# Kernel tuning notes

Measured on AMD Instinct MI355X. Metric: run time of the kernel, lower is better.

## Reference

```python
import jax, jax.numpy as jnp
import numpy as np

B, NP, N, C, H = 16, 512, 1024, 1024, 16
HD = C // H
HID = 4 * C
EPS = 1e-5


def _layernorm(x, g, b):
    mu = jnp.mean(x, axis=-1, keepdims=True)
    var = jnp.mean(jnp.square(x - mu), axis=-1, keepdims=True)
    return (x - mu) * jax.lax.rsqrt(var + EPS) * g + b


def setup_inputs() -> dict:
    key = jax.random.key(0)
    ks = jax.random.split(key, 12)
    x = jax.random.normal(ks[0], (B, NP, C), dtype=jnp.float32)
    cache_k = jax.random.normal(ks[1], (B, H, N, HD), dtype=jnp.float32)
    cache_v = jax.random.normal(ks[2], (B, H, N, HD), dtype=jnp.float32)
    # update_mask: exactly NP active (to-be-updated) token slots per batch row
    scores = jax.random.uniform(ks[3], (B, N))
    top = jnp.argsort(scores, axis=1)[:, :NP]
    update_mask = jnp.zeros((B, N), dtype=bool).at[jnp.arange(B)[:, None], top].set(True)
    s = 0.02
    qkv_w = jax.random.normal(ks[4], (C, 3 * C), dtype=jnp.float32) * s
    qkv_b = jnp.zeros((3 * C,), dtype=jnp.float32)
    proj_w = jax.random.normal(ks[5], (C, C), dtype=jnp.float32) * s
    proj_b = jnp.zeros((C,), dtype=jnp.float32)
    n1_g = jnp.ones((C,), dtype=jnp.float32)
    n1_b = jnp.zeros((C,), dtype=jnp.float32)
    n2_g = jnp.ones((C,), dtype=jnp.float32)
    n2_b = jnp.zeros((C,), dtype=jnp.float32)
    fc1_w = jax.random.normal(ks[6], (C, HID), dtype=jnp.float32) * s
    fc1_b = jnp.zeros((HID,), dtype=jnp.float32)
    fc2_w = jax.random.normal(ks[7], (HID, C), dtype=jnp.float32) * s
    fc2_b = jnp.zeros((C,), dtype=jnp.float32)
    return dict(x=x, cache_k=cache_k, cache_v=cache_v, update_mask=update_mask,
                qkv_w=qkv_w, qkv_b=qkv_b, proj_w=proj_w, proj_b=proj_b,
                n1_g=n1_g, n1_b=n1_b, n2_g=n2_g, n2_b=n2_b,
                fc1_w=fc1_w, fc1_b=fc1_b, fc2_w=fc2_w, fc2_b=fc2_b)


def reference(x, cache_k, cache_v, update_mask, qkv_w, qkv_b, proj_w, proj_b,
              n1_g, n1_b, n2_g, n2_b, fc1_w, fc1_b, fc2_w, fc2_b):
    Bq, Np, Cd = x.shape
    h = _layernorm(x, n1_g, n1_b)
    qkv = (h @ qkv_w + qkv_b).reshape(Bq, Np, 3, H, HD)
    q, k, v = jnp.moveaxis(qkv, 2, 0)               # each [B, Np, H, HD]
    q = jnp.swapaxes(q, 1, 2)                       # [B, H, Np, HD]
    k = jnp.swapaxes(k, 1, 2)
    v = jnp.swapaxes(v, 1, 2)
    # masked_scatter_: i-th new token -> i-th masked slot (row-uniform mask count)
    idx = jnp.argsort(jnp.logical_not(update_mask), axis=1)[:, :Np]  # [B, Np]
    k_full = jax.vmap(lambda c, i, kn: c.at[:, i, :].set(kn))(cache_k, idx, k)
    v_full = jax.vmap(lambda c, i, vn: c.at[:, i, :].set(vn))(cache_v, idx, v)
    scale = HD ** -0.5
    attn = jnp.einsum('bhqd,bhkd->bhqk', q * scale, k_full)  # [B,H,Np,N]
    attn = jax.nn.softmax(attn, axis=-1)
    o = jnp.einsum('bhqk,bhkd->bhqd', attn, v_full)
    o = jnp.swapaxes(o, 1, 2).reshape(Bq, Np, Cd)
    o = o @ proj_w + proj_b
    x = x + o
    h2 = _layernorm(x, n2_g, n2_b)
    mlp = jax.nn.gelu(h2 @ fc1_w + fc1_b, approximate=False) @ fc2_w + fc2_b
    return x + mlp
```

## Files before the change

kernel.cpp:

```cpp
#include <hip/hip_runtime.h>
#include <hip/hip_bf16.h>
#include <math.h>

#define Bd   16
#define NPd  512
#define Nd   1024
#define Cd   1024
#define Hd   16
#define HDd  64
#define HIDd 4096
#define EPSd 1e-5f

typedef unsigned short u16;
typedef __bf16 bf16x8 __attribute__((ext_vector_type(8)));
typedef float  f32x4  __attribute__((ext_vector_type(4)));

__device__ __forceinline__ u16 f2bf(float f) {
    unsigned int u = __builtin_bit_cast(unsigned int, f);
    u = u + 0x7fffu + ((u >> 16) & 1u);
    return (u16)(u >> 16);
}

__device__ __forceinline__ void async_load16(const void* g, void* l) {
    __builtin_amdgcn_global_load_lds(
        (const __attribute__((address_space(1))) void*)(uintptr_t)g,
        (__attribute__((address_space(3))) void*)(unsigned int)(uintptr_t)l,
        16, 0, 0);
}

__global__ __launch_bounds__(256) void build_src(const void* __restrict__ mask_raw,
                                                 int* __restrict__ src) {
    const int b = blockIdx.x;
    const int t = threadIdx.x;
    const unsigned char* m8 = (const unsigned char*)mask_raw;
    const int* m32 = (const int*)mask_raw;

    int c = 0;
    #pragma unroll
    for (int i = 0; i < 4; i++) c += (m8[b * Nd + t * 4 + i] != 0) ? 1 : 0;
    #pragma unroll
    for (int off = 1; off < 64; off <<= 1) c += __shfl_xor(c, off);
    __shared__ int warr[4];
    if ((t & 63) == 0) warr[t >> 6] = c;
    __syncthreads();
    const int c8 = warr[0] + warr[1] + warr[2] + warr[3];
    const bool use8 = (c8 == NPd);

    int f[4];
    #pragma unroll
    for (int i = 0; i < 4; i++) {
        const int n = t * 4 + i;
        f[i] = use8 ? (m8[b * Nd + n] != 0) : (m32[b * Nd + n] != 0);
    }
    const int loc = f[0] + f[1] + f[2] + f[3];

    int sc_ = loc;
    #pragma unroll
    for (int off = 1; off < 64; off <<= 1) {
        const int u = __shfl_up(sc_, off);
        if ((t & 63) >= off) sc_ += u;
    }
    __shared__ int wtot[4];
    __syncthreads();
    if ((t & 63) == 63) wtot[t >> 6] = sc_;
    __syncthreads();
    int base = 0;
    for (int w = 0; w < (t >> 6); w++) base += wtot[w];

    int run = base + sc_ - loc;
    #pragma unroll
    for (int i = 0; i < 4; i++) {
        const int n = t * 4 + i;
        src[b * Nd + n] = f[i] ? run : -1;
        run += f[i];
    }
}

__global__ __launch_bounds__(256) void ln_kernel(const float* __restrict__ x,
                                                 const float* __restrict__ g,
                                                 const float* __restrict__ bb,
                                                 u16* __restrict__ out) {
    const int row = blockIdx.x;
    const int t = threadIdx.x;
    const float* xr = x + (size_t)row * Cd;
    const float4 v = *(const float4*)(xr + t * 4);
    float s = v.x + v.y + v.z + v.w;
    float q = v.x * v.x + v.y * v.y + v.z * v.z + v.w * v.w;
    #pragma unroll
    for (int off = 1; off < 64; off <<= 1) {
        s += __shfl_xor(s, off);
        q += __shfl_xor(q, off);
    }
    __shared__ float ss[4], qq[4];
    if ((t & 63) == 0) { ss[t >> 6] = s; qq[t >> 6] = q; }
    __syncthreads();
    s = ss[0] + ss[1] + ss[2] + ss[3];
    q = qq[0] + qq[1] + qq[2] + qq[3];
    const float mu = s * (1.0f / Cd);
    const float var = q * (1.0f / Cd) - mu * mu;
    const float rs = rsqrtf(var + EPSd);
    const float4 gv = *(const float4*)(g + t * 4);
    const float4 bv = *(const float4*)(bb + t * 4);
    ushort4 r;
    r.x = f2bf((v.x - mu) * rs * gv.x + bv.x);
    r.y = f2bf((v.y - mu) * rs * gv.y + bv.y);
    r.z = f2bf((v.z - mu) * rs * gv.z + bv.z);
    r.w = f2bf((v.w - mu) * rs * gv.w + bv.w);
    *(ushort4*)(out + (size_t)row * Cd + t * 4) = r;
}

__global__ __launch_bounds__(256) void conv_t(const float* __restrict__ W,
                                              u16* __restrict__ Wt,
                                              int K, int N) {
    __shared__ float tile[32][33];
    const int k0 = blockIdx.y * 32;
    const int n0 = blockIdx.x * 32;
    const int t = threadIdx.x;
    const int row = t >> 3, c4 = (t & 7) * 4;
    const float4 v = *(const float4*)(W + (size_t)(k0 + row) * N + n0 + c4);
    tile[row][c4 + 0] = v.x;
    tile[row][c4 + 1] = v.y;
    tile[row][c4 + 2] = v.z;
    tile[row][c4 + 3] = v.w;
    __syncthreads();
    ushort4 o;
    o.x = f2bf(tile[c4 + 0][row]);
    o.y = f2bf(tile[c4 + 1][row]);
    o.z = f2bf(tile[c4 + 2][row]);
    o.w = f2bf(tile[c4 + 3][row]);
    *(ushort4*)(Wt + (size_t)(n0 + row) * K + k0 + c4) = o;
}

template <int EPI, typename OUT_T>
__global__ __launch_bounds__(256) void gemm_mfma(const u16* __restrict__ A,
                                                 const u16* __restrict__ Wt,
                                                 const float* __restrict__ bias,
                                                 const float* __restrict__ res,
                                                 OUT_T* __restrict__ out,
                                                 int K, int Nn) {
    __shared__ u16 As[128 * 32];
    __shared__ u16 Bs[128 * 32];

    const int t = threadIdx.x;
    const int L = t & 63;
    const int w = t >> 6;
    const int wm = w >> 1, wn = w & 1;
    const int m0 = blockIdx.y * 128;
    const int n0 = blockIdx.x * 128;

    const int srow = 32 * w + (L >> 2);
    const int scol = (L & 3) * 8;
    const u16* ap0 = A  + (size_t)(m0 + srow) * K + scol;
    const u16* ap1 = ap0 + (size_t)16 * K;
    const u16* bp0 = Wt + (size_t)(n0 + srow) * K + scol;
    const u16* bp1 = bp0 + (size_t)16 * K;
    u16* alds0 = As + w * 1024;
    u16* alds1 = alds0 + 512;
    u16* blds0 = Bs + w * 1024;
    u16* blds1 = blds0 + 512;

    f32x4 acc[4][4];
    const f32x4 zero = {0.f, 0.f, 0.f, 0.f};
    #pragma unroll
    for (int i = 0; i < 4; i++)
        #pragma unroll
        for (int j = 0; j < 4; j++) acc[i][j] = zero;

    const int frag_off = (L & 15) * 32 + (L >> 4) * 8;

    for (int kt = 0; kt < K; kt += 32) {
        __syncthreads();
        async_load16(ap0 + kt, alds0);
        async_load16(ap1 + kt, alds1);
        async_load16(bp0 + kt, blds0);
        async_load16(bp1 + kt, blds1);
        __syncthreads();

        bf16x8 a[4], b[4];
        #pragma unroll
        for (int i = 0; i < 4; i++) {
            a[i] = *(const bf16x8*)&As[(wm * 64 + i * 16) * 32 + frag_off];
            b[i] = *(const bf16x8*)&Bs[(wn * 64 + i * 16) * 32 + frag_off];
        }
        #pragma unroll
        for (int i = 0; i < 4; i++)
            #pragma unroll
            for (int j = 0; j < 4; j++)
                acc[i][j] = __builtin_amdgcn_mfma_f32_16x16x32_bf16(a[i], b[j], acc[i][j], 0, 0, 0);
    }

    const int cn = n0 + wn * 64 + (L & 15);
    const int cm = m0 + wm * 64 + (L >> 4) * 4;
    #pragma unroll
    for (int i = 0; i < 4; i++) {
        #pragma unroll
        for (int j = 0; j < 4; j++) {
            const int nn = cn + j * 16;
            const float bv = bias[nn];
            #pragma unroll
            for (int r = 0; r < 4; r++) {
                const int mm = cm + i * 16 + r;
                float v = acc[i][j][r] + bv;
                if (EPI == 2) v = 0.5f * v * (1.0f + erff(v * 0.70710678118654752f));
                if (EPI == 1) v += res[(size_t)mm * Nn + nn];
                if constexpr (sizeof(OUT_T) == 2) out[(size_t)mm * Nn + nn] = (OUT_T)f2bf(v);
                else out[(size_t)mm * Nn + nn] = v;
            }
        }
    }
}

__global__ __launch_bounds__(256) void kv_cast(const u16* __restrict__ qkv,
                                               const float* __restrict__ ck,
                                               const float* __restrict__ cv,
                                               const int* __restrict__ srcArr,
                                               u16* __restrict__ Kb,
                                               u16* __restrict__ Vtb) {
    const int id = blockIdx.x;
    const int nt = id & 15, hh = (id >> 4) & 15, b = id >> 8;
    const int t = threadIdx.x;
    __shared__ u16 Vl[64][72];

    const int row = t >> 2;
    const int dd = (t & 3) * 16;
    const int n = nt * 64 + row;
    const int sidx = srcArr[b * Nd + n];

    u16 kv16[16], vv16[16];
    if (sidx >= 0) {
        const u16* kp = qkv + (size_t)(b * NPd + sidx) * 3072 + Cd + hh * 64 + dd;
        const u16* vp = kp + Cd;
        *(ulonglong2*)&kv16[0] = *(const ulonglong2*)kp;
        *(ulonglong2*)&kv16[8] = *(const ulonglong2*)(kp + 8);
        *(ulonglong2*)&vv16[0] = *(const ulonglong2*)vp;
        *(ulonglong2*)&vv16[8] = *(const ulonglong2*)(vp + 8);
    } else {
        const float* kp = ck + ((size_t)((b * Hd + hh) * Nd + n)) * HDd + dd;
        const float* vp = cv + ((size_t)((b * Hd + hh) * Nd + n)) * HDd + dd;
        #pragma unroll
        for (int c = 0; c < 4; c++) {
            const float4 kc4 = *(const float4*)(kp + c * 4);
            const float4 vc4 = *(const float4*)(vp + c * 4);
            kv16[c * 4 + 0] = f2bf(kc4.x); kv16[c * 4 + 1] = f2bf(kc4.y);
            kv16[c * 4 + 2] = f2bf(kc4.z); kv16[c * 4 + 3] = f2bf(kc4.w);
            vv16[c * 4 + 0] = f2bf(vc4.x); vv16[c * 4 + 1] = f2bf(vc4.y);
            vv16[c * 4 + 2] = f2bf(vc4.z); vv16[c * 4 + 3] = f2bf(vc4.w);
        }
    }

    u16* ko = Kb + ((size_t)((b * Hd + hh) * Nd + n)) * HDd + dd;
    *(ulonglong2*)ko = *(ulonglong2*)&kv16[0];
    *(ulonglong2*)(ko + 8) = *(ulonglong2*)&kv16[8];

    #pragma unroll
    for (int i = 0; i < 16; i++) Vl[row][dd + i] = vv16[i];
    __syncthreads();

    const int d = t >> 2, nc = (t & 3) * 16;
    u16 ov[16];
    #pragma unroll
    for (int i = 0; i < 16; i++) ov[i] = Vl[nc + i][d];
    u16* vo = Vtb + ((size_t)((b * Hd + hh) * HDd + d)) * Nd + nt * 64 + nc;
    *(ulonglong2*)vo = *(ulonglong2*)&ov[0];
    *(ulonglong2*)(vo + 8) = *(ulonglong2*)&ov[8];
}

__global__ __launch_bounds__(256) void attn_mfma(const u16* __restrict__ qkv,
                                                 const u16* __restrict__ Kb,
                                                 const u16* __restrict__ Vtb,
                                                 u16* __restrict__ attno) {
    const int bh = blockIdx.x;
    const int qt = blockIdx.y;
    const int b = bh >> 4, hh = bh & 15;
    const int t = threadIdx.x;
    const int L = t & 63;
    const int w = t >> 6;

    __shared__ u16 Qs[4096];
    __shared__ u16 Ks[4096];
    __shared__ u16 Vs[4096];
    __shared__ u16 Ps[4][16 * 72];

    const size_t kbase = (size_t)((b * Hd + hh) * Nd) * HDd;
    const size_t vbase = (size_t)((b * Hd + hh) * HDd) * Nd;

    #pragma unroll
    for (int j = 0; j < 2; j++) {
        const int row = 16 * w + 8 * j + (L >> 3);
        const int ch = (L & 7) ^ (row & 7);
        const u16* g = qkv + (size_t)(b * NPd + qt * 64 + row) * 3072 + hh * 64 + ch * 8;
        async_load16(g, Qs + (16 * w + 8 * j) * 64);
    }

    f32x4 acc[4];
    const f32x4 zero = {0.f, 0.f, 0.f, 0.f};
    #pragma unroll
    for (int nb = 0; nb < 4; nb++) acc[nb] = zero;
    float m_run[4] = {-INFINITY, -INFINITY, -INFINITY, -INFINITY};
    float l_run[4] = {0.f, 0.f, 0.f, 0.f};

    for (int kt = 0; kt < 16; kt++) {
        __syncthreads();
        #pragma unroll
        for (int j = 0; j < 2; j++) {
            const int row = 16 * w + 8 * j + (L >> 3);
            const int ch = (L & 7) ^ (row & 7);
            async_load16(Kb + kbase + (size_t)(kt * 64 + row) * 64 + ch * 8,
                         Ks + (16 * w + 8 * j) * 64);
            async_load16(Vtb + vbase + (size_t)row * Nd + kt * 64 + ch * 8,
                         Vs + (16 * w + 8 * j) * 64);
        }
        __syncthreads();

        const int qrow = 16 * w + (L & 15);
        const bf16x8 aq0 = *(const bf16x8*)&Qs[qrow * 64 + (((L >> 4)     ^ (L & 7)) * 8)];
        const bf16x8 aq1 = *(const bf16x8*)&Qs[qrow * 64 + (((4 + (L >> 4)) ^ (L & 7)) * 8)];

        f32x4 s[4];
        #pragma unroll
        for (int kb = 0; kb < 4; kb++) {
            const int krow = kb * 16 + (L & 15);
            const bf16x8 bk0 = *(const bf16x8*)&Ks[krow * 64 + (((L >> 4)     ^ (L & 7)) * 8)];
            const bf16x8 bk1 = *(const bf16x8*)&Ks[krow * 64 + (((4 + (L >> 4)) ^ (L & 7)) * 8)];
            s[kb] = __builtin_amdgcn_mfma_f32_16x16x32_bf16(aq0, bk0, zero, 0, 0, 0);
            s[kb] = __builtin_amdgcn_mfma_f32_16x16x32_bf16(aq1, bk1, s[kb], 0, 0, 0);
        }

        float al[4];
        float pb[4][4];
        #pragma unroll
        for (int r = 0; r < 4; r++) {
            float m = fmaxf(fmaxf(s[0][r], s[1][r]), fmaxf(s[2][r], s[3][r])) * 0.125f;
            m = fmaxf(m, __shfl_xor(m, 1));
            m = fmaxf(m, __shfl_xor(m, 2));
            m = fmaxf(m, __shfl_xor(m, 4));
            m = fmaxf(m, __shfl_xor(m, 8));
            const float mn = fmaxf(m_run[r], m);
            al[r] = __expf(m_run[r] - mn);
            m_run[r] = mn;
        }
        float ps[4] = {0.f, 0.f, 0.f, 0.f};
        #pragma unroll
        for (int kb = 0; kb < 4; kb++)
            #pragma unroll
            for (int r = 0; r < 4; r++) {
                const float p = __expf(s[kb][r] * 0.125f - m_run[r]);
                pb[kb][r] = p;
                ps[r] += p;
            }
        #pragma unroll
        for (int r = 0; r < 4; r++) {
            ps[r] += __shfl_xor(ps[r], 1);
            ps[r] += __shfl_xor(ps[r], 2);
            ps[r] += __shfl_xor(ps[r], 4);
            ps[r] += __shfl_xor(ps[r], 8);
            l_run[r] = l_run[r] * al[r] + ps[r];
        }
        #pragma unroll
        for (int nb = 0; nb < 4; nb++)
            #pragma unroll
            for (int r = 0; r < 4; r++) acc[nb][r] *= al[r];

        u16* pw = &Ps[w][0];
        #pragma unroll
        for (int kb = 0; kb < 4; kb++)
            #pragma unroll
            for (int r = 0; r < 4; r++)
                pw[((L >> 4) * 4 + r) * 72 + kb * 16 + (L & 15)] = f2bf(pb[kb][r]);

        const bf16x8 ap0 = *(const bf16x8*)&Ps[w][(L & 15) * 72 +      (L >> 4) * 8];
        const bf16x8 ap1 = *(const bf16x8*)&Ps[w][(L & 15) * 72 + 32 + (L >> 4) * 8];
        #pragma unroll
        for (int nb = 0; nb < 4; nb++) {
            const int drow = nb * 16 + (L & 15);
            const bf16x8 bv0 = *(const bf16x8*)&Vs[drow * 64 + (((L >> 4)     ^ (L & 7)) * 8)];
            const bf16x8 bv1 = *(const bf16x8*)&Vs[drow * 64 + (((4 + (L >> 4)) ^ (L & 7)) * 8)];
            acc[nb] = __builtin_amdgcn_mfma_f32_16x16x32_bf16(ap0, bv0, acc[nb], 0, 0, 0);
            acc[nb] = __builtin_amdgcn_mfma_f32_16x16x32_bf16(ap1, bv1, acc[nb], 0, 0, 0);
        }
    }

    float inv[4];
    #pragma unroll
    for (int r = 0; r < 4; r++) inv[r] = 1.0f / l_run[r];
    #pragma unroll
    for (int nb = 0; nb < 4; nb++)
        #pragma unroll
        for (int r = 0; r < 4; r++) {
            const int q = qt * 64 + w * 16 + (L >> 4) * 4 + r;
            const int d = nb * 16 + (L & 15);
            attno[(size_t)(b * NPd + q) * Cd + hh * 64 + d] = f2bf(acc[nb][r] * inv[r]);
        }
}

extern "C" void kernel_launch(void* const* d_in, const int* in_sizes, int n_in,
                              void* d_out, int out_size, void* d_ws, size_t ws_size,
                              hipStream_t stream) {
    const float* x       = (const float*)d_in[0];
    const float* cache_k = (const float*)d_in[1];
    const float* cache_v = (const float*)d_in[2];
    const void*  mask    = d_in[3];
    const float* qkv_w   = (const float*)d_in[4];
    const float* qkv_b   = (const float*)d_in[5];
    const float* proj_w  = (const float*)d_in[6];
    const float* proj_b  = (const float*)d_in[7];
    const float* n1_g    = (const float*)d_in[8];
    const float* n1_b    = (const float*)d_in[9];
    const float* n2_g    = (const float*)d_in[10];
    const float* n2_b    = (const float*)d_in[11];
    const float* fc1_w   = (const float*)d_in[12];
    const float* fc1_b   = (const float*)d_in[13];
    const float* fc2_w   = (const float*)d_in[14];
    const float* fc2_b   = (const float*)d_in[15];
    float* out = (float*)d_out;

    const size_t MR = (size_t)Bd * NPd;
    char* ws = (char*)d_ws;
    int*   srcArr = (int*)ws;
    float* x2     = (float*)(ws + 65536);
    u16*   h      = (u16*)(x2 + MR * Cd);
    u16*   attno  = h + MR * Cd;
    u16*   qkv    = attno + MR * Cd;
    u16*   Kb     = qkv + MR * 3 * Cd;
    u16*   Vtb    = Kb + (size_t)Bd * Hd * Nd * HDd;
    u16*   m1     = qkv;
    u16*   qkv_wt = Vtb + (size_t)Bd * Hd * Nd * HDd;
    u16*   proj_wt= qkv_wt + (size_t)3 * Cd * Cd;
    u16*   fc1_wt = proj_wt + (size_t)Cd * Cd;
    u16*   fc2_wt = fc1_wt + (size_t)Cd * HIDd;

    build_src<<<Bd, 256, 0, stream>>>(mask, srcArr);
    conv_t<<<dim3(3 * Cd / 32, Cd / 32),  256, 0, stream>>>(qkv_w,  qkv_wt,  Cd,   3 * Cd);
    conv_t<<<dim3(Cd / 32, Cd / 32),      256, 0, stream>>>(proj_w, proj_wt, Cd,   Cd);
    conv_t<<<dim3(HIDd / 32, Cd / 32),    256, 0, stream>>>(fc1_w,  fc1_wt,  Cd,   HIDd);
    conv_t<<<dim3(Cd / 32, HIDd / 32),    256, 0, stream>>>(fc2_w,  fc2_wt,  HIDd, Cd);

    ln_kernel<<<MR, 256, 0, stream>>>(x, n1_g, n1_b, h);
    gemm_mfma<0, u16><<<dim3(3 * Cd / 128, MR / 128), 256, 0, stream>>>(h, qkv_wt, qkv_b, nullptr, qkv, Cd, 3 * Cd);
    kv_cast<<<Bd * Hd * (Nd / 64), 256, 0, stream>>>(qkv, cache_k, cache_v, srcArr, Kb, Vtb);
    attn_mfma<<<dim3(Bd * Hd, NPd / 64), 256, 0, stream>>>(qkv, Kb, Vtb, attno);
    gemm_mfma<1, float><<<dim3(Cd / 128, MR / 128), 256, 0, stream>>>(attno, proj_wt, proj_b, x, x2, Cd, Cd);
    ln_kernel<<<MR, 256, 0, stream>>>(x2, n2_g, n2_b, h);
    gemm_mfma<2, u16><<<dim3(HIDd / 128, MR / 128), 256, 0, stream>>>(h, fc1_wt, fc1_b, nullptr, m1, Cd, HIDd);
    gemm_mfma<1, float><<<dim3(Cd / 128, MR / 128), 256, 0, stream>>>(m1, fc2_wt, fc2_b, x2, out, HIDd, Cd);
}
```

Baseline: 703.3 us.

## Split-K the proj and fc2 GEMMs and fuse partial reduction with LayerNorm

The projection and fc2 GEMMs are launched with two K-slices, so each gets twice as many blocks, and write fp32 partials into reused workspace buffers. A new reduce kernel adds the two partials, bias and residual, and for the projection also computes LN2 in the same pass, replacing the separate ln_kernel. This aims to improve CU occupancy on the narrow N=1024 GEMMs. In exchange it writes and reads extra fp32 partial buffers and aliases them onto dead workspace regions.

```diff
diff --git a/kernel.cpp b/kernel.cpp
--- a/kernel.cpp
+++ b/kernel.cpp
@@ -208,6 +208,143 @@
             }
         }
     }
+}
+
+__global__ __launch_bounds__(256) void gemm_mfma_sk(const u16* __restrict__ A,
+                                                    const u16* __restrict__ Wt,
+                                                    float* __restrict__ part0,
+                                                    float* __restrict__ part1,
+                                                    int Kstride, int KL, int Nn) {
+    __shared__ u16 As[128 * 32];
+    __shared__ u16 Bs[128 * 32];
+
+    const int t = threadIdx.x;
+    const int L = t & 63;
+    const int w = t >> 6;
+    const int wm = w >> 1, wn = w & 1;
+    const int m0 = blockIdx.y * 128;
+    const int n0 = blockIdx.x * 128;
+    const int z = blockIdx.z;
+    float* outp = z ? part1 : part0;
+    const int k0 = z * KL;
+
+    const int srow = 32 * w + (L >> 2);
+    const int scol = (L & 3) * 8;
+    const u16* ap0 = A  + (size_t)(m0 + srow) * Kstride + k0 + scol;
+    const u16* ap1 = ap0 + (size_t)16 * Kstride;
+    const u16* bp0 = Wt + (size_t)(n0 + srow) * Kstride + k0 + scol;
+    const u16* bp1 = bp0 + (size_t)16 * Kstride;
+    u16* alds0 = As + w * 1024;
+    u16* alds1 = alds0 + 512;
+    u16* blds0 = Bs + w * 1024;
+    u16* blds1 = blds0 + 512;
+
+    f32x4 acc[4][4];
+    const f32x4 zero = {0.f, 0.f, 0.f, 0.f};
+    #pragma unroll
+    for (int i = 0; i < 4; i++)
+        #pragma unroll
+        for (int j = 0; j < 4; j++) acc[i][j] = zero;
+
+    const int frag_off = (L & 15) * 32 + (L >> 4) * 8;
+
+    for (int kt = 0; kt < KL; kt += 32) {
+        __syncthreads();
+        async_load16(ap0 + kt, alds0);
+        async_load16(ap1 + kt, alds1);
+        async_load16(bp0 + kt, blds0);
+        async_load16(bp1 + kt, blds1);
+        __syncthreads();
+
+        bf16x8 a[4], b[4];
+        #pragma unroll
+        for (int i = 0; i < 4; i++) {
+            a[i] = *(const bf16x8*)&As[(wm * 64 + i * 16) * 32 + frag_off];
+            b[i] = *(const bf16x8*)&Bs[(wn * 64 + i * 16) * 32 + frag_off];
+        }
+        #pragma unroll
+        for (int i = 0; i < 4; i++)
+            #pragma unroll
+            for (int j = 0; j < 4; j++)
+                acc[i][j] = __builtin_amdgcn_mfma_f32_16x16x32_bf16(a[i], b[j], acc[i][j], 0, 0, 0);
+    }
+
+    const int cn = n0 + wn * 64 + (L & 15);
+    const int cm = m0 + wm * 64 + (L >> 4) * 4;
+    #pragma unroll
+    for (int i = 0; i < 4; i++)
+        #pragma unroll
+        for (int j = 0; j < 4; j++)
+            #pragma unroll
+            for (int r = 0; r < 4; r++)
+                outp[(size_t)(cm + i * 16 + r) * Nn + cn + j * 16] = acc[i][j][r];
+}
+
+__global__ __launch_bounds__(256) void reduce_ln(const float* __restrict__ p0,
+                                                 const float* __restrict__ p1,
+                                                 const float* __restrict__ bias,
+                                                 const float* __restrict__ xres,
+                                                 const float* __restrict__ g,
+                                                 const float* __restrict__ bb,
+                                                 float* __restrict__ x2,
+                                                 u16* __restrict__ hout) {
+    const int row = blockIdx.x;
+    const int t = threadIdx.x;
+    const size_t off = (size_t)row * Cd + t * 4;
+    const float4 a = *(const float4*)(p0 + off);
+    const float4 b = *(const float4*)(p1 + off);
+    const float4 bi = *(const float4*)(bias + t * 4);
+    const float4 rr = *(const float4*)(xres + off);
+    float4 v;
+    v.x = a.x + b.x + bi.x + rr.x;
+    v.y = a.y + b.y + bi.y + rr.y;
+    v.z = a.z + b.z + bi.z + rr.z;
+    v.w = a.w + b.w + bi.w + rr.w;
+    *(float4*)(x2 + off) = v;
+
+    float s = v.x + v.y + v.z + v.w;
+    float q = v.x * v.x + v.y * v.y + v.z * v.z + v.w * v.w;
+    #pragma unroll
+    for (int o = 1; o < 64; o <<= 1) {
+        s += __shfl_xor(s, o);
+        q += __shfl_xor(q, o);
+    }
+    __shared__ float ss[4], qq[4];
+    if ((t & 63) == 0) { ss[t >> 6] = s; qq[t >> 6] = q; }
+    __syncthreads();
+    s = ss[0] + ss[1] + ss[2] + ss[3];
+    q = qq[0] + qq[1] + qq[2] + qq[3];
+    const float mu = s * (1.0f / Cd);
+    const float var = q * (1.0f / Cd) - mu * mu;
+    const float rs = rsqrtf(var + EPSd);
+    const float4 gv = *(const float4*)(g + t * 4);
+    const float4 bv = *(const float4*)(bb + t * 4);
+    ushort4 r;
+    r.x = f2bf((v.x - mu) * rs * gv.x + bv.x);
+    r.y = f2bf((v.y - mu) * rs * gv.y + bv.y);
+    r.z = f2bf((v.z - mu) * rs * gv.z + bv.z);
+    r.w = f2bf((v.w - mu) * rs * gv.w + bv.w);
+    *(ushort4*)(hout + off) = r;
+}
+
+__global__ __launch_bounds__(256) void reduce_out(const float* __restrict__ p0,
+                                                  const float* __restrict__ p1,
+                                                  const float* __restrict__ bias,
+                                                  const float* __restrict__ xres,
+                                                  float* __restrict__ out) {
+    const int row = blockIdx.x;
+    const int t = threadIdx.x;
+    const size_t off = (size_t)row * Cd + t * 4;
+    const float4 a = *(const float4*)(p0 + off);
+    const float4 b = *(const float4*)(p1 + off);
+    const float4 bi = *(const float4*)(bias + t * 4);
+    const float4 rr = *(const float4*)(xres + off);
+    float4 v;
+    v.x = a.x + b.x + bi.x + rr.x;
+    v.y = a.y + b.y + bi.y + rr.y;
+    v.z = a.z + b.z + bi.z + rr.z;
+    v.w = a.w + b.w + bi.w + rr.w;
+    *(float4*)(out + off) = v;
 }
 
 __global__ __launch_bounds__(256) void kv_cast(const u16* __restrict__ qkv,
@@ -429,6 +566,11 @@
     u16*   fc1_wt = proj_wt + (size_t)Cd * Cd;
     u16*   fc2_wt = fc1_wt + (size_t)Cd * HIDd;
 
+    float* pa0 = (float*)qkv;
+    float* pa1 = (float*)Vtb;
+    float* pb0 = (float*)h;
+    float* pb1 = (float*)Vtb;
+
     build_src<<<Bd, 256, 0, stream>>>(mask, srcArr);
     conv_t<<<dim3(3 * Cd / 32, Cd / 32),  256, 0, stream>>>(qkv_w,  qkv_wt,  Cd,   3 * Cd);
     conv_t<<<dim3(Cd / 32, Cd / 32),      256, 0, stream>>>(proj_w, proj_wt, Cd,   Cd);
@@ -439,8 +581,12 @@
     gemm_mfma<0, u16><<<dim3(3 * Cd / 128, MR / 128), 256, 0, stream>>>(h, qkv_wt, qkv_b, nullptr, qkv, Cd, 3 * Cd);
     kv_cast<<<Bd * Hd * (Nd / 64), 256, 0, stream>>>(qkv, cache_k, cache_v, srcArr, Kb, Vtb);
     attn_mfma<<<dim3(Bd * Hd, NPd / 64), 256, 0, stream>>>(qkv, Kb, Vtb, attno);
-    gemm_mfma<1, float><<<dim3(Cd / 128, MR / 128), 256, 0, stream>>>(attno, proj_wt, proj_b, x, x2, Cd, Cd);
-    ln_kernel<<<MR, 256, 0, stream>>>(x2, n2_g, n2_b, h);
+
+    gemm_mfma_sk<<<dim3(Cd / 128, MR / 128, 2), 256, 0, stream>>>(attno, proj_wt, pa0, pa1, Cd, 512, Cd);
+    reduce_ln<<<MR, 256, 0, stream>>>(pa0, pa1, proj_b, x, n2_g, n2_b, x2, h);
+
     gemm_mfma<2, u16><<<dim3(HIDd / 128, MR / 128), 256, 0, stream>>>(h, fc1_wt, fc1_b, nullptr, m1, Cd, HIDd);
-    gemm_mfma<1, float><<<dim3(Cd / 128, MR / 128), 256, 0, stream>>>(m1, fc2_wt, fc2_b, x2, out, HIDd, Cd);
-}
+
+    gemm_mfma_sk<<<dim3(Cd / 128, MR / 128, 2), 256, 0, stream>>>(m1, fc2_wt, pb0, pb1, HIDd, 2048, Cd);
+    reduce_out<<<MR, 256, 0, stream>>>(pb0, pb1, fc2_b, x2, out);
+}
```

New measurement: 750.6 us. 6.7% more time.
